# Kernel optimization log

Measured on AMD Instinct MI355X. Metric: run time of the kernel, lower is better.

Reference implementation:

```python
import jax, jax.numpy as jnp
import numpy as np
import math

B, S, D, H, DFF = 4, 2048, 1024, 16, 4096
DK = D // H
EPS = 1e-5


def setup_inputs() -> dict:
    key = jax.random.key(0)
    ks = jax.random.split(key, 12)
    sc = 0.02
    inp = {
        "x": jax.random.normal(ks[0], (B, S, D), dtype=jnp.float32),
        "mask": jnp.ones((B, 1, 1, S), dtype=jnp.int32),
        "Wq": jax.random.normal(ks[1], (D, D), jnp.float32) * sc,
        "bq": jnp.zeros((D,), jnp.float32),
        "Wk": jax.random.normal(ks[2], (D, D), jnp.float32) * sc,
        "bk": jnp.zeros((D,), jnp.float32),
        "Wv": jax.random.normal(ks[3], (D, D), jnp.float32) * sc,
        "bv": jnp.zeros((D,), jnp.float32),
        "Wo": jax.random.normal(ks[4], (D, D), jnp.float32) * sc,
        "bo": jnp.zeros((D,), jnp.float32),
        "ln1_g": jnp.ones((D,), jnp.float32),
        "ln1_b": jnp.zeros((D,), jnp.float32),
        "W1": jax.random.normal(ks[5], (D, DFF), jnp.float32) * sc,
        "b1": jnp.zeros((DFF,), jnp.float32),
        "W2": jax.random.normal(ks[6], (DFF, D), jnp.float32) * sc,
        "b2": jnp.zeros((D,), jnp.float32),
        "ln2_g": jnp.ones((D,), jnp.float32),
        "ln2_b": jnp.zeros((D,), jnp.float32),
    }
    return inp


def _layer_norm(x, g, b):
    m = jnp.mean(x, axis=-1, keepdims=True)
    v = jnp.mean(jnp.square(x - m), axis=-1, keepdims=True)
    return (x - m) * jax.lax.rsqrt(v + EPS) * g + b


def reference(x, mask, Wq, bq, Wk, bk, Wv, bv, Wo, bo,
              ln1_g, ln1_b, W1, b1, W2, b2, ln2_g, ln2_b):
    b_, s_, d_ = x.shape
    h_, dk_ = H, DK
    # --- pre-LN attention sublayer ---
    hidden = _layer_norm(x, ln1_g, ln1_b)
    q = (hidden @ Wq + bq).reshape(b_, s_, h_, dk_).transpose(0, 2, 1, 3)  # [B,H,S,dk]
    k = (hidden @ Wk + bk).reshape(b_, s_, h_, dk_).transpose(0, 2, 1, 3)  # [B,H,S,dk]
    # NOTE: original code passes value=key (the value projection is dead code),
    # so K is used both as keys and as values. Reproduced faithfully.
    scores = jnp.einsum("bhqd,bhkd->bhqk", q, k) / math.sqrt(dk_)  # [B,H,S,S]
    scores = jnp.where(mask == 0, jnp.float32(-1e9), scores)
    p_attn = jax.nn.softmax(scores, axis=-1)
    attn_out = jnp.einsum("bhqk,bhkd->bhqd", p_attn, k)  # values == k
    attn_out = attn_out.transpose(0, 2, 1, 3).reshape(b_, s_, d_)
    attn_out = attn_out @ Wo + bo
    x = x + attn_out  # residual (dropout is identity in eval)
    # --- pre-LN FFN sublayer ---
    hidden2 = _layer_norm(x, ln2_g, ln2_b)
    ff = jax.nn.gelu(hidden2 @ W1 + b1, approximate=False) @ W2 + b2
    return x + ff
```

## Files before the change

### kernel.cpp

```cpp
#include <hip/hip_runtime.h>
#include <hip/hip_bf16.h>
#include <math.h>

#define B_   4
#define S_   2048
#define D_   1024
#define H_   16
#define DK_  64
#define DFF_ 4096
#define M_   (B_*S_)

typedef __bf16 bf16;
typedef bf16 bf16x8 __attribute__((ext_vector_type(8)));
typedef bf16 bf16x4 __attribute__((ext_vector_type(4)));
typedef float f32x4 __attribute__((ext_vector_type(4)));

__device__ __forceinline__ void g2lds16(const void* g, void* l) {
  __builtin_amdgcn_global_load_lds(
      (__attribute__((address_space(1))) void*)(void*)g,
      (__attribute__((address_space(3))) void*)l, 16, 0, 0);
}

__device__ __forceinline__ void* swzp(char* base, int row, int byteofs) {
  return base + row * 128 + (byteofs ^ ((row & 7) << 4));
}

__global__ void tcast(const float* __restrict__ W, bf16* __restrict__ Wt,
                      int K, int N) {
  __shared__ float t[32][33];
  int n0 = blockIdx.x * 32, k0 = blockIdx.y * 32;
  int tx = threadIdx.x, ty = threadIdx.y;
#pragma unroll
  for (int i = 0; i < 4; ++i)
    t[ty + i*8][tx] = W[(size_t)(k0 + ty + i*8) * N + n0 + tx];
  __syncthreads();
#pragma unroll
  for (int i = 0; i < 4; ++i)
    Wt[(size_t)(n0 + ty + i*8) * K + k0 + tx] = (bf16)t[tx][ty + i*8];
}

__global__ __launch_bounds__(256)
void ktrans(const bf16* __restrict__ Kt, bf16* __restrict__ KT) {
  __shared__ bf16 t[64][72];
  const int bh = blockIdx.y, s0 = blockIdx.x * 64, tid = threadIdx.x;
  const bf16* src = Kt + (size_t)bh * S_ * DK_;
  bf16* dst = KT + (size_t)bh * DK_ * S_;
#pragma unroll
  for (int i = 0; i < 2; ++i) {
    int c = tid * 2 + i;
    int r = c >> 3, col = (c & 7) * 8;
    *(bf16x8*)&t[r][col] = *(const bf16x8*)&src[(size_t)(s0 + r) * 64 + col];
  }
  __syncthreads();
  const int d = tid >> 2, sc = (tid & 3) * 16;
  bf16x8 v0, v1;
#pragma unroll
  for (int j = 0; j < 8; ++j) { v0[j] = t[sc + j][d]; v1[j] = t[sc + 8 + j][d]; }
  *(bf16x8*)&dst[(size_t)d * S_ + s0 + sc] = v0;
  *(bf16x8*)&dst[(size_t)d * S_ + s0 + sc + 8] = v1;
}

__global__ __launch_bounds__(256)
void ln_fwd(const float* __restrict__ x, const float* __restrict__ g,
            const float* __restrict__ be, bf16* __restrict__ out) {
  int row = blockIdx.x, tid = threadIdx.x;
  const float4 v = *(const float4*)&x[(size_t)row * D_ + tid * 4];
  float s = v.x + v.y + v.z + v.w;
  float q = v.x*v.x + v.y*v.y + v.z*v.z + v.w*v.w;
#pragma unroll
  for (int d = 32; d; d >>= 1) { s += __shfl_down(s, d); q += __shfl_down(q, d); }
  __shared__ float red[8];
  int wave = tid >> 6, lane = tid & 63;
  if (lane == 0) { red[wave*2] = s; red[wave*2+1] = q; }
  __syncthreads();
  float ts = red[0] + red[2] + red[4] + red[6];
  float tq = red[1] + red[3] + red[5] + red[7];
  float mean = ts * (1.0f / D_);
  float var  = tq * (1.0f / D_) - mean * mean;
  float rstd = rsqrtf(var + 1e-5f);
  const float4 gg = *(const float4*)&g[tid * 4];
  const float4 bb = *(const float4*)&be[tid * 4];
  bf16x4 ov;
  ov[0] = (bf16)((v.x - mean) * rstd * gg.x + bb.x);
  ov[1] = (bf16)((v.y - mean) * rstd * gg.y + bb.y);
  ov[2] = (bf16)((v.z - mean) * rstd * gg.z + bb.z);
  ov[3] = (bf16)((v.w - mean) * rstd * gg.w + bb.w);
  *(bf16x4*)&out[(size_t)row * D_ + tid * 4] = ov;
}

template <int EPI>
__global__ __launch_bounds__(256)
void gemm_bt(const bf16* __restrict__ A, const bf16* __restrict__ Bt,
             int M, int N, int K,
             const float* __restrict__ bias, const float* __restrict__ resid,
             float scale, float* __restrict__ outf, bf16* __restrict__ outb) {
  __shared__ __align__(16) bf16 As[128 * 32];
  __shared__ __align__(16) bf16 Bs[128 * 32];
  const int tid = threadIdx.x;
  const int wave = tid >> 6, lane = tid & 63;
  const int wr = wave >> 1, wc = wave & 1;

  const int gx = gridDim.x, nwg = gx * gridDim.y;
  int wg = blockIdx.y * gx + blockIdx.x;
  wg = (wg & 7) * (nwg >> 3) + (wg >> 3);
  const long arow = (long)(wg / gx) * 128;
  const long bcol = (long)(wg % gx) * 128;

  f32x4 acc[4][4] = {};

  const int c0 = wave * 2, c1 = wave * 2 + 1;
  const int srow0 = c0 * 16 + (lane >> 2);
  const int srow1 = c1 * 16 + (lane >> 2);
  const int scol = (lane & 3) * 8;
  const int l15 = lane & 15, kof = (lane >> 4) * 8;

  for (int k0 = 0; k0 < K; k0 += 32) {
    g2lds16(A  + (arow + srow0) * (long)K + k0 + scol, &As[c0 * 512]);
    g2lds16(A  + (arow + srow1) * (long)K + k0 + scol, &As[c1 * 512]);
    g2lds16(Bt + (bcol + srow0) * (long)K + k0 + scol, &Bs[c0 * 512]);
    g2lds16(Bt + (bcol + srow1) * (long)K + k0 + scol, &Bs[c1 * 512]);
    __syncthreads();
    bf16x8 a[4], b[4];
#pragma unroll
    for (int i = 0; i < 4; ++i)
      a[i] = *(const bf16x8*)&As[(wr * 64 + i * 16 + l15) * 32 + kof];
#pragma unroll
    for (int i = 0; i < 4; ++i)
      b[i] = *(const bf16x8*)&Bs[(wc * 64 + i * 16 + l15) * 32 + kof];
#pragma unroll
    for (int mi = 0; mi < 4; ++mi)
#pragma unroll
      for (int ni = 0; ni < 4; ++ni)
        acc[mi][ni] = __builtin_amdgcn_mfma_f32_16x16x32_bf16(
            a[mi], b[ni], acc[mi][ni], 0, 0, 0);
    __syncthreads();
  }

#pragma unroll
  for (int mi = 0; mi < 4; ++mi) {
#pragma unroll
    for (int ni = 0; ni < 4; ++ni) {
#pragma unroll
      for (int j = 0; j < 4; ++j) {
        long row = arow + wr * 64 + mi * 16 + (lane >> 4) * 4 + j;
        long col = bcol + wc * 64 + ni * 16 + l15;
        float v = acc[mi][ni][j];
        if constexpr (EPI == 0) {
          int bb = (int)(row >> 11), ss = (int)(row & 2047);
          int hh = (int)(col >> 6), dd = (int)(col & 63);
          size_t idx = (((size_t)(bb * H_ + hh)) * S_ + ss) * DK_ + dd;
          outb[idx] = (bf16)((v + bias[col]) * scale);
        } else if constexpr (EPI == 1) {
          size_t idx = (size_t)row * N + col;
          outf[idx] = v + bias[col] + resid[idx];
        } else {
          size_t idx = (size_t)row * N + col;
          float t = v + bias[col];
          outb[idx] = (bf16)(0.5f * t * (1.0f + erff(t * 0.70710678118654752f)));
        }
      }
    }
  }
}

__global__ __launch_bounds__(256)
void attn_fwd(const bf16* __restrict__ Q, const bf16* __restrict__ Kk,
              const bf16* __restrict__ KT, const int* __restrict__ mask,
              bf16* __restrict__ O) {
  __shared__ __align__(16) char Kl[64 * 128];
  __shared__ __align__(16) char Vl[64 * 128];
  __shared__ __align__(16) char Pl[4][16 * 128];

  const int tid = threadIdx.x, wave = tid >> 6, lane = tid & 63;
  const int bh = blockIdx.y, b = bh >> 4, h = bh & 15;
  const int q0 = blockIdx.x * 64;
  const int l15 = lane & 15, q4 = lane >> 4;

  const bf16* Qp = Q  + (size_t)bh * S_ * DK_;
  const bf16* Kp = Kk + (size_t)bh * S_ * DK_;
  const bf16* Tp = KT + (size_t)bh * DK_ * S_;

  const int qrow = q0 + wave * 16 + l15;
  const bf16x8 qf0 = *(const bf16x8*)&Qp[(size_t)qrow * 64 + q4 * 8];
  const bf16x8 qf1 = *(const bf16x8*)&Qp[(size_t)qrow * 64 + 32 + q4 * 8];

  const int c0 = tid * 2, c1 = tid * 2 + 1;
  const int sr0 = c0 >> 3, sb0 = c0 & 7;
  const int sr1 = c1 >> 3, sb1 = c1 & 7;

  f32x4 o[4] = {};
  float m_r[4], l_r[4];
#pragma unroll
  for (int j = 0; j < 4; ++j) { m_r[j] = -__builtin_inff(); l_r[j] = 0.f; }

  for (int k0 = 0; k0 < S_; k0 += 64) {
    bf16x8 a0 = *(const bf16x8*)&Kp[(size_t)(k0 + sr0) * 64 + sb0 * 8];
    bf16x8 a1 = *(const bf16x8*)&Kp[(size_t)(k0 + sr1) * 64 + sb1 * 8];
    bf16x8 t0 = *(const bf16x8*)&Tp[(size_t)sr0 * S_ + k0 + sb0 * 8];
    bf16x8 t1 = *(const bf16x8*)&Tp[(size_t)sr1 * S_ + k0 + sb1 * 8];
    *(bf16x8*)swzp(Kl, sr0, sb0 * 16) = a0;
    *(bf16x8*)swzp(Kl, sr1, sb1 * 16) = a1;
    *(bf16x8*)swzp(Vl, sr0, sb0 * 16) = t0;
    *(bf16x8*)swzp(Vl, sr1, sb1 * 16) = t1;
    __syncthreads();

    f32x4 s[4];
#pragma unroll
    for (int nt = 0; nt < 4; ++nt) {
      bf16x8 kf0 = *(const bf16x8*)swzp(Kl, nt * 16 + l15, q4 * 16);
      bf16x8 kf1 = *(const bf16x8*)swzp(Kl, nt * 16 + l15, 64 + q4 * 16);
      f32x4 z = {};
      z     = __builtin_amdgcn_mfma_f32_16x16x32_bf16(qf0, kf0, z, 0, 0, 0);
      s[nt] = __builtin_amdgcn_mfma_f32_16x16x32_bf16(qf1, kf1, z, 0, 0, 0);
    }
#pragma unroll
    for (int nt = 0; nt < 4; ++nt) {
      int mv = mask[b * S_ + k0 + nt * 16 + l15];
      if (mv == 0) {
#pragma unroll
        for (int j = 0; j < 4; ++j) s[nt][j] = -1e9f;
      }
    }
    float rmax[4], rsum[4], sf[4];
#pragma unroll
    for (int j = 0; j < 4; ++j)
      rmax[j] = fmaxf(fmaxf(s[0][j], s[1][j]), fmaxf(s[2][j], s[3][j]));
#pragma unroll
    for (int d = 1; d < 16; d <<= 1)
#pragma unroll
      for (int j = 0; j < 4; ++j)
        rmax[j] = fmaxf(rmax[j], __shfl_xor(rmax[j], d));
#pragma unroll
    for (int j = 0; j < 4; ++j) {
      float mnew = fmaxf(m_r[j], rmax[j]);
      sf[j] = __builtin_amdgcn_exp2f(m_r[j] - mnew);
      m_r[j] = mnew;
      rsum[j] = 0.f;
    }
#pragma unroll
    for (int nt = 0; nt < 4; ++nt)
#pragma unroll
      for (int j = 0; j < 4; ++j) {
        float p = __builtin_amdgcn_exp2f(s[nt][j] - m_r[j]);
        s[nt][j] = p;
        rsum[j] += p;
      }
#pragma unroll
    for (int d = 1; d < 16; d <<= 1)
#pragma unroll
      for (int j = 0; j < 4; ++j) rsum[j] += __shfl_xor(rsum[j], d);
#pragma unroll
    for (int j = 0; j < 4; ++j) l_r[j] = l_r[j] * sf[j] + rsum[j];
#pragma unroll
    for (int nf = 0; nf < 4; ++nf)
#pragma unroll
      for (int j = 0; j < 4; ++j) o[nf][j] *= sf[j];

#pragma unroll
    for (int nt = 0; nt < 4; ++nt)
#pragma unroll
      for (int j = 0; j < 4; ++j)
        *(bf16*)swzp(Pl[wave], q4 * 4 + j, (nt * 16 + l15) * 2) =
            (bf16)s[nt][j];

    const bf16x8 pf0 = *(const bf16x8*)swzp(Pl[wave], l15, q4 * 16);
    const bf16x8 pf1 = *(const bf16x8*)swzp(Pl[wave], l15, 64 + q4 * 16);
#pragma unroll
    for (int nf = 0; nf < 4; ++nf) {
      bf16x8 vf0 = *(const bf16x8*)swzp(Vl, nf * 16 + l15, q4 * 16);
      bf16x8 vf1 = *(const bf16x8*)swzp(Vl, nf * 16 + l15, 64 + q4 * 16);
      o[nf] = __builtin_amdgcn_mfma_f32_16x16x32_bf16(pf0, vf0, o[nf], 0, 0, 0);
      o[nf] = __builtin_amdgcn_mfma_f32_16x16x32_bf16(pf1, vf1, o[nf], 0, 0, 0);
    }
    __syncthreads();
  }

#pragma unroll
  for (int nf = 0; nf < 4; ++nf)
#pragma unroll
    for (int j = 0; j < 4; ++j) {
      int row = q0 + wave * 16 + q4 * 4 + j;
      int col = h * 64 + nf * 16 + l15;
      O[((size_t)b * S_ + row) * D_ + col] = (bf16)(o[nf][j] / l_r[j]);
    }
}

extern "C" void kernel_launch(void* const* d_in, const int* in_sizes, int n_in,
                              void* d_out, int out_size, void* d_ws, size_t ws_size,
                              hipStream_t stream) {
  const float* x    = (const float*)d_in[0];
  const int*   mask = (const int*)d_in[1];
  const float* Wq   = (const float*)d_in[2];
  const float* bq   = (const float*)d_in[3];
  const float* Wk   = (const float*)d_in[4];
  const float* bk   = (const float*)d_in[5];
  const float* Wo   = (const float*)d_in[8];
  const float* bo   = (const float*)d_in[9];
  const float* ln1g = (const float*)d_in[10];
  const float* ln1b = (const float*)d_in[11];
  const float* W1   = (const float*)d_in[12];
  const float* b1   = (const float*)d_in[13];
  const float* W2   = (const float*)d_in[14];
  const float* b2   = (const float*)d_in[15];
  const float* ln2g = (const float*)d_in[16];
  const float* ln2b = (const float*)d_in[17];
  float* out = (float*)d_out;

  char* w = (char*)d_ws;
  auto alloc = [&](size_t bytes) {
    void* p = (void*)w;
    w += (bytes + 255) & ~(size_t)255;
    return p;
  };
  bf16* xln  = (bf16*)alloc((size_t)M_ * D_ * 2);
  bf16* WqT  = (bf16*)alloc((size_t)D_ * D_ * 2);
  bf16* WkT  = (bf16*)alloc((size_t)D_ * D_ * 2);
  bf16* WoT  = (bf16*)alloc((size_t)D_ * D_ * 2);
  bf16* W1T  = (bf16*)alloc((size_t)D_ * DFF_ * 2);
  bf16* W2T  = (bf16*)alloc((size_t)D_ * DFF_ * 2);
  bf16* Qt   = (bf16*)alloc((size_t)M_ * D_ * 2);
  bf16* Kt   = (bf16*)alloc((size_t)M_ * D_ * 2);
  bf16* KTt  = (bf16*)alloc((size_t)M_ * D_ * 2);
  bf16* attn = (bf16*)alloc((size_t)M_ * D_ * 2);
  float* x2  = (float*)alloc((size_t)M_ * D_ * 4);
  bf16* h2   = (bf16*)alloc((size_t)M_ * D_ * 2);
  bf16* act  = (bf16*)alloc((size_t)M_ * DFF_ * 2);

  dim3 blk32(32, 8);
  tcast<<<dim3(32, 32),  blk32, 0, stream>>>(Wq, WqT, D_, D_);
  tcast<<<dim3(32, 32),  blk32, 0, stream>>>(Wk, WkT, D_, D_);
  tcast<<<dim3(32, 32),  blk32, 0, stream>>>(Wo, WoT, D_, D_);
  tcast<<<dim3(128, 32), blk32, 0, stream>>>(W1, W1T, D_, DFF_);
  tcast<<<dim3(32, 128), blk32, 0, stream>>>(W2, W2T, DFF_, D_);

  ln_fwd<<<M_, 256, 0, stream>>>(x, ln1g, ln1b, xln);

  gemm_bt<0><<<dim3(8, 64), 256, 0, stream>>>(xln, WqT, M_, D_, D_, bq, nullptr,
                                              0.125f * 1.4426950408889634f,
                                              nullptr, Qt);
  gemm_bt<0><<<dim3(8, 64), 256, 0, stream>>>(xln, WkT, M_, D_, D_, bk, nullptr,
                                              1.0f, nullptr, Kt);

  ktrans<<<dim3(S_ / 64, B_ * H_), 256, 0, stream>>>(Kt, KTt);

  attn_fwd<<<dim3(S_ / 64, B_ * H_), 256, 0, stream>>>(Qt, Kt, KTt, mask, attn);

  gemm_bt<1><<<dim3(8, 64), 256, 0, stream>>>(attn, WoT, M_, D_, D_, bo, x,
                                              1.0f, x2, nullptr);

  ln_fwd<<<M_, 256, 0, stream>>>(x2, ln2g, ln2b, h2);

  gemm_bt<2><<<dim3(32, 64), 256, 0, stream>>>(h2, W1T, M_, DFF_, D_, b1, nullptr,
                                               1.0f, nullptr, act);
  gemm_bt<1><<<dim3(8, 64), 256, 0, stream>>>(act, W2T, M_, D_, DFF_, b2, x2,
                                              1.0f, out, nullptr);
}
```

Baseline: 682.5 us.

## Fuse weight casts and Q/K GEMMs; prefetch and lazily rescale attention softmax

Merges the five weight transpose-cast launches into one kernel and combines the Q and K projections into a single GEMM over a concatenated weight, with an epilogue that writes to two outputs. In attention, the next K/V tile is prefetched into registers, the mask fixup is skipped when no element in the tile is masked, the row sum is computed with an MFMA against a vector of ones instead of shuffles, and rescaling of the output is skipped unless the running max grows by more than 8 (in the log2 domain). These cut launch count and per-tile ALU, shuffle and sync work, at the cost of more register pressure and unnormalised exp values of up to 2^8 before the final divide.

```diff
diff --git a/kernel.cpp b/kernel.cpp
--- a/kernel.cpp
+++ b/kernel.cpp
@@ -25,18 +25,28 @@
   return base + row * 128 + (byteofs ^ ((row & 7) << 4));
 }
 
-__global__ void tcast(const float* __restrict__ W, bf16* __restrict__ Wt,
-                      int K, int N) {
+__global__ void tcast_all(const float* __restrict__ Wq, const float* __restrict__ Wk,
+                          const float* __restrict__ Wo, const float* __restrict__ W1,
+                          const float* __restrict__ W2,
+                          bf16* __restrict__ WqkT, bf16* __restrict__ WoT,
+                          bf16* __restrict__ W1T, bf16* __restrict__ W2T) {
   __shared__ float t[32][33];
-  int n0 = blockIdx.x * 32, k0 = blockIdx.y * 32;
+  int bid = blockIdx.x;
+  const float* src; bf16* dst; int K, N, bx, by;
+  if (bid < 1024)      { src = Wq; dst = WqkT;            K = 1024; N = 1024; bx = bid & 31;  by = bid >> 5; }
+  else if (bid < 2048) { bid -= 1024; src = Wk; dst = WqkT + 1024 * 1024; K = 1024; N = 1024; bx = bid & 31;  by = bid >> 5; }
+  else if (bid < 3072) { bid -= 2048; src = Wo; dst = WoT; K = 1024; N = 1024; bx = bid & 31;  by = bid >> 5; }
+  else if (bid < 7168) { bid -= 3072; src = W1; dst = W1T; K = 1024; N = 4096; bx = bid & 127; by = bid >> 7; }
+  else                 { bid -= 7168; src = W2; dst = W2T; K = 4096; N = 1024; bx = bid & 31;  by = bid >> 5; }
+  int n0 = bx * 32, k0 = by * 32;
   int tx = threadIdx.x, ty = threadIdx.y;
 #pragma unroll
   for (int i = 0; i < 4; ++i)
-    t[ty + i*8][tx] = W[(size_t)(k0 + ty + i*8) * N + n0 + tx];
+    t[ty + i*8][tx] = src[(size_t)(k0 + ty + i*8) * N + n0 + tx];
   __syncthreads();
 #pragma unroll
   for (int i = 0; i < 4; ++i)
-    Wt[(size_t)(n0 + ty + i*8) * K + k0 + tx] = (bf16)t[tx][ty + i*8];
+    dst[(size_t)(n0 + ty + i*8) * K + k0 + tx] = (bf16)t[tx][ty + i*8];
 }
 
 __global__ __launch_bounds__(256)
@@ -92,8 +102,10 @@
 __global__ __launch_bounds__(256)
 void gemm_bt(const bf16* __restrict__ A, const bf16* __restrict__ Bt,
              int M, int N, int K,
-             const float* __restrict__ bias, const float* __restrict__ resid,
-             float scale, float* __restrict__ outf, bf16* __restrict__ outb) {
+             const float* __restrict__ bias, const float* __restrict__ bias2,
+             const float* __restrict__ resid, float scale,
+             float* __restrict__ outf, bf16* __restrict__ outb,
+             bf16* __restrict__ outb2) {
   __shared__ __align__(16) bf16 As[128 * 32];
   __shared__ __align__(16) bf16 Bs[128 * 32];
   const int tid = threadIdx.x;
@@ -147,9 +159,10 @@
         float v = acc[mi][ni][j];
         if constexpr (EPI == 0) {
           int bb = (int)(row >> 11), ss = (int)(row & 2047);
-          int hh = (int)(col >> 6), dd = (int)(col & 63);
+          int hh = (int)(col >> 6) & 15, dd = (int)(col & 63);
           size_t idx = (((size_t)(bb * H_ + hh)) * S_ + ss) * DK_ + dd;
-          outb[idx] = (bf16)((v + bias[col]) * scale);
+          if (col < 1024) outb[idx]  = (bf16)((v + bias[col]) * scale);
+          else            outb2[idx] = (bf16)(v + bias2[col - 1024]);
         } else if constexpr (EPI == 1) {
           size_t idx = (size_t)row * N + col;
           outf[idx] = v + bias[col] + resid[idx];
@@ -188,21 +201,47 @@
   const int sr0 = c0 >> 3, sb0 = c0 & 7;
   const int sr1 = c1 >> 3, sb1 = c1 & 7;
 
+  int poff[16];
+#pragma unroll
+  for (int nt = 0; nt < 4; ++nt)
+#pragma unroll
+    for (int j = 0; j < 4; ++j) {
+      int r = q4 * 4 + j;
+      poff[nt * 4 + j] = r * 128 + ((((nt * 16 + l15) * 2)) ^ ((r & 7) << 4));
+    }
+
+  bf16x8 onesv;
+#pragma unroll
+  for (int i = 0; i < 8; ++i) onesv[i] = (bf16)1.0f;
+
   f32x4 o[4] = {};
-  float m_r[4], l_r[4];
-#pragma unroll
-  for (int j = 0; j < 4; ++j) { m_r[j] = -__builtin_inff(); l_r[j] = 0.f; }
+  f32x4 ol = {};
+  float m_r[4];
+#pragma unroll
+  for (int j = 0; j < 4; ++j) m_r[j] = -__builtin_inff();
+
+  bf16x8 a0 = *(const bf16x8*)&Kp[(size_t)sr0 * 64 + sb0 * 8];
+  bf16x8 a1 = *(const bf16x8*)&Kp[(size_t)sr1 * 64 + sb1 * 8];
+  bf16x8 t0 = *(const bf16x8*)&Tp[(size_t)sr0 * S_ + sb0 * 8];
+  bf16x8 t1 = *(const bf16x8*)&Tp[(size_t)sr1 * S_ + sb1 * 8];
 
   for (int k0 = 0; k0 < S_; k0 += 64) {
-    bf16x8 a0 = *(const bf16x8*)&Kp[(size_t)(k0 + sr0) * 64 + sb0 * 8];
-    bf16x8 a1 = *(const bf16x8*)&Kp[(size_t)(k0 + sr1) * 64 + sb1 * 8];
-    bf16x8 t0 = *(const bf16x8*)&Tp[(size_t)sr0 * S_ + k0 + sb0 * 8];
-    bf16x8 t1 = *(const bf16x8*)&Tp[(size_t)sr1 * S_ + k0 + sb1 * 8];
     *(bf16x8*)swzp(Kl, sr0, sb0 * 16) = a0;
     *(bf16x8*)swzp(Kl, sr1, sb1 * 16) = a1;
     *(bf16x8*)swzp(Vl, sr0, sb0 * 16) = t0;
     *(bf16x8*)swzp(Vl, sr1, sb1 * 16) = t1;
     __syncthreads();
+
+    const int nk = k0 + 64;
+    if (nk < S_) {
+      a0 = *(const bf16x8*)&Kp[(size_t)(nk + sr0) * 64 + sb0 * 8];
+      a1 = *(const bf16x8*)&Kp[(size_t)(nk + sr1) * 64 + sb1 * 8];
+      t0 = *(const bf16x8*)&Tp[(size_t)sr0 * S_ + nk + sb0 * 8];
+      t1 = *(const bf16x8*)&Tp[(size_t)sr1 * S_ + nk + sb1 * 8];
+    }
+
+    const int mv = mask[b * S_ + k0 + lane];
+    const bool anyz = __any(mv == 0);
 
     f32x4 s[4];
 #pragma unroll
@@ -213,58 +252,55 @@
       z     = __builtin_amdgcn_mfma_f32_16x16x32_bf16(qf0, kf0, z, 0, 0, 0);
       s[nt] = __builtin_amdgcn_mfma_f32_16x16x32_bf16(qf1, kf1, z, 0, 0, 0);
     }
-#pragma unroll
-    for (int nt = 0; nt < 4; ++nt) {
-      int mv = mask[b * S_ + k0 + nt * 16 + l15];
-      if (mv == 0) {
-#pragma unroll
-        for (int j = 0; j < 4; ++j) s[nt][j] = -1e9f;
+    if (anyz) {
+#pragma unroll
+      for (int nt = 0; nt < 4; ++nt) {
+        int m2 = mask[b * S_ + k0 + nt * 16 + l15];
+        if (m2 == 0) {
+#pragma unroll
+          for (int j = 0; j < 4; ++j) s[nt][j] = -1e9f;
+        }
       }
     }
-    float rmax[4], rsum[4], sf[4];
+
+    float tm[4];
 #pragma unroll
     for (int j = 0; j < 4; ++j)
-      rmax[j] = fmaxf(fmaxf(s[0][j], s[1][j]), fmaxf(s[2][j], s[3][j]));
+      tm[j] = fmaxf(fmaxf(s[0][j], s[1][j]), fmaxf(s[2][j], s[3][j]));
 #pragma unroll
     for (int d = 1; d < 16; d <<= 1)
 #pragma unroll
       for (int j = 0; j < 4; ++j)
-        rmax[j] = fmaxf(rmax[j], __shfl_xor(rmax[j], d));
-#pragma unroll
-    for (int j = 0; j < 4; ++j) {
-      float mnew = fmaxf(m_r[j], rmax[j]);
-      sf[j] = __builtin_amdgcn_exp2f(m_r[j] - mnew);
-      m_r[j] = mnew;
-      rsum[j] = 0.f;
-    }
+        tm[j] = fmaxf(tm[j], __shfl_xor(tm[j], d));
+
+    bool ok = true;
+#pragma unroll
+    for (int j = 0; j < 4; ++j) ok = ok && (tm[j] <= m_r[j] + 8.0f);
+    if (!__all(ok)) {
+#pragma unroll
+      for (int j = 0; j < 4; ++j) {
+        float mn = fmaxf(m_r[j], tm[j]);
+        float sf = __builtin_amdgcn_exp2f(m_r[j] - mn);
+        m_r[j] = mn;
+        ol[j] *= sf;
+#pragma unroll
+        for (int nf = 0; nf < 4; ++nf) o[nf][j] *= sf;
+      }
+    }
+
 #pragma unroll
     for (int nt = 0; nt < 4; ++nt)
 #pragma unroll
-      for (int j = 0; j < 4; ++j) {
-        float p = __builtin_amdgcn_exp2f(s[nt][j] - m_r[j]);
-        s[nt][j] = p;
-        rsum[j] += p;
-      }
-#pragma unroll
-    for (int d = 1; d < 16; d <<= 1)
-#pragma unroll
-      for (int j = 0; j < 4; ++j) rsum[j] += __shfl_xor(rsum[j], d);
-#pragma unroll
-    for (int j = 0; j < 4; ++j) l_r[j] = l_r[j] * sf[j] + rsum[j];
-#pragma unroll
-    for (int nf = 0; nf < 4; ++nf)
-#pragma unroll
-      for (int j = 0; j < 4; ++j) o[nf][j] *= sf[j];
-
-#pragma unroll
-    for (int nt = 0; nt < 4; ++nt)
-#pragma unroll
       for (int j = 0; j < 4; ++j)
-        *(bf16*)swzp(Pl[wave], q4 * 4 + j, (nt * 16 + l15) * 2) =
-            (bf16)s[nt][j];
+        *(bf16*)(&Pl[wave][0] + poff[nt * 4 + j]) =
+            (bf16)__builtin_amdgcn_exp2f(s[nt][j] - m_r[j]);
 
     const bf16x8 pf0 = *(const bf16x8*)swzp(Pl[wave], l15, q4 * 16);
     const bf16x8 pf1 = *(const bf16x8*)swzp(Pl[wave], l15, 64 + q4 * 16);
+
+    ol = __builtin_amdgcn_mfma_f32_16x16x32_bf16(pf0, onesv, ol, 0, 0, 0);
+    ol = __builtin_amdgcn_mfma_f32_16x16x32_bf16(pf1, onesv, ol, 0, 0, 0);
+
 #pragma unroll
     for (int nf = 0; nf < 4; ++nf) {
       bf16x8 vf0 = *(const bf16x8*)swzp(Vl, nf * 16 + l15, q4 * 16);
@@ -281,7 +317,7 @@
     for (int j = 0; j < 4; ++j) {
       int row = q0 + wave * 16 + q4 * 4 + j;
       int col = h * 64 + nf * 16 + l15;
-      O[((size_t)b * S_ + row) * D_ + col] = (bf16)(o[nf][j] / l_r[j]);
+      O[((size_t)b * S_ + row) * D_ + col] = (bf16)(o[nf][j] / ol[j]);
     }
 }
 
@@ -313,8 +349,7 @@
     return p;
   };
   bf16* xln  = (bf16*)alloc((size_t)M_ * D_ * 2);
-  bf16* WqT  = (bf16*)alloc((size_t)D_ * D_ * 2);
-  bf16* WkT  = (bf16*)alloc((size_t)D_ * D_ * 2);
+  bf16* WqkT = (bf16*)alloc((size_t)2 * D_ * D_ * 2);
   bf16* WoT  = (bf16*)alloc((size_t)D_ * D_ * 2);
   bf16* W1T  = (bf16*)alloc((size_t)D_ * DFF_ * 2);
   bf16* W2T  = (bf16*)alloc((size_t)D_ * DFF_ * 2);
@@ -326,32 +361,29 @@
   bf16* h2   = (bf16*)alloc((size_t)M_ * D_ * 2);
   bf16* act  = (bf16*)alloc((size_t)M_ * DFF_ * 2);
 
-  dim3 blk32(32, 8);
-  tcast<<<dim3(32, 32),  blk32, 0, stream>>>(Wq, WqT, D_, D_);
-  tcast<<<dim3(32, 32),  blk32, 0, stream>>>(Wk, WkT, D_, D_);
-  tcast<<<dim3(32, 32),  blk32, 0, stream>>>(Wo, WoT, D_, D_);
-  tcast<<<dim3(128, 32), blk32, 0, stream>>>(W1, W1T, D_, DFF_);
-  tcast<<<dim3(32, 128), blk32, 0, stream>>>(W2, W2T, DFF_, D_);
+  tcast_all<<<11264, dim3(32, 8), 0, stream>>>(Wq, Wk, Wo, W1, W2,
+                                               WqkT, WoT, W1T, W2T);
 
   ln_fwd<<<M_, 256, 0, stream>>>(x, ln1g, ln1b, xln);
 
-  gemm_bt<0><<<dim3(8, 64), 256, 0, stream>>>(xln, WqT, M_, D_, D_, bq, nullptr,
-                                              0.125f * 1.4426950408889634f,
-                                              nullptr, Qt);
-  gemm_bt<0><<<dim3(8, 64), 256, 0, stream>>>(xln, WkT, M_, D_, D_, bk, nullptr,
-                                              1.0f, nullptr, Kt);
+  gemm_bt<0><<<dim3(16, 64), 256, 0, stream>>>(
+      xln, WqkT, M_, 2048, 1024, bq, bk, nullptr,
+      0.125f * 1.4426950408889634f, nullptr, Qt, Kt);
 
   ktrans<<<dim3(S_ / 64, B_ * H_), 256, 0, stream>>>(Kt, KTt);
 
   attn_fwd<<<dim3(S_ / 64, B_ * H_), 256, 0, stream>>>(Qt, Kt, KTt, mask, attn);
 
-  gemm_bt<1><<<dim3(8, 64), 256, 0, stream>>>(attn, WoT, M_, D_, D_, bo, x,
-                                              1.0f, x2, nullptr);
+  gemm_bt<1><<<dim3(8, 64), 256, 0, stream>>>(attn, WoT, M_, 1024, 1024,
+                                              bo, nullptr, x, 1.0f,
+                                              x2, nullptr, nullptr);
 
   ln_fwd<<<M_, 256, 0, stream>>>(x2, ln2g, ln2b, h2);
 
-  gemm_bt<2><<<dim3(32, 64), 256, 0, stream>>>(h2, W1T, M_, DFF_, D_, b1, nullptr,
-                                               1.0f, nullptr, act);
-  gemm_bt<1><<<dim3(8, 64), 256, 0, stream>>>(act, W2T, M_, D_, DFF_, b2, x2,
-                                              1.0f, out, nullptr);
-}
+  gemm_bt<2><<<dim3(32, 64), 256, 0, stream>>>(h2, W1T, M_, 4096, 1024,
+                                               b1, nullptr, nullptr, 1.0f,
+                                               nullptr, act, nullptr);
+  gemm_bt<1><<<dim3(8, 64), 256, 0, stream>>>(act, W2T, M_, 1024, 4096,
+                                              b2, nullptr, x2, 1.0f,
+                                              out, nullptr, nullptr);
+}
```

New measurement: 661.5 us. -3.1%, faster.
